# Performance work log

Measured on AMD Instinct MI355X. Metric: run time of the kernel, lower is better.

The kernel has to match this reference:

```python
import jax, jax.numpy as jnp
import numpy as np

N_E = 100000       # entities
N_R = 1000         # relations
N_CLASSES = 20000  # class_index.max() + 1
E = 1000000        # edges (triples)
E_HIDDEN = 256
C_HIDDEN = 128
R_HIDDEN = 128
NEG_SLOPE = 0.01   # F.leaky_relu default


def leaky_relu(x):
    return jnp.where(x >= 0, x, NEG_SLOPE * x)


def segment_softmax(x, idx, num_segments):
    # torch_geometric-style scatter softmax over segments given by idx
    m = jax.ops.segment_max(x, idx, num_segments=num_segments)
    ex = jnp.exp(x - m[idx])
    s = jax.ops.segment_sum(ex, idx, num_segments=num_segments)
    return ex / (s[idx] + 1e-16)


def setup_inputs() -> dict:
    key = jax.random.key(0)
    ks = jax.random.split(key, 20)
    inv_c = 1.0 / np.sqrt(C_HIDDEN)
    inv_r = 1.0 / np.sqrt(R_HIDDEN)
    inv_e = 1.0 / np.sqrt(E_HIDDEN)
    inp = {
        "x_e": jax.random.normal(ks[0], (N_E, E_HIDDEN), jnp.float32),
        "edge_index": jax.random.randint(ks[1], (2, E), 0, N_E),
        "rel": jax.random.randint(ks[2], (E,), 0, N_R),
        "triple_num": jax.random.randint(ks[3], (E,), 0, N_E),
        "r_emb": jax.random.normal(ks[4], (N_R, R_HIDDEN), jnp.float32),
        "class_index": jax.random.randint(ks[5], (E,), 0, N_CLASSES),
        "head_class": jax.random.randint(ks[6], (N_CLASSES,), 0, N_E),
        # attention projection vectors (Linear(c_hidden,1,bias=False) weights)
        "a_h1": jax.random.normal(ks[7], (C_HIDDEN,), jnp.float32) * inv_c,
        "a_h2": jax.random.normal(ks[8], (C_HIDDEN,), jnp.float32) * inv_c,
        "a_h3": jax.random.normal(ks[9], (C_HIDDEN,), jnp.float32) * inv_c,
        "a_h4": jax.random.normal(ks[10], (C_HIDDEN,), jnp.float32) * inv_c,
        "a_t1": jax.random.normal(ks[11], (C_HIDDEN,), jnp.float32) * inv_c,
        "a_t2": jax.random.normal(ks[12], (C_HIDDEN,), jnp.float32) * inv_c,
        "a_t3": jax.random.normal(ks[13], (C_HIDDEN,), jnp.float32) * inv_c,
        "a_r1": jax.random.normal(ks[14], (R_HIDDEN,), jnp.float32) * inv_r,
        "a_r2": jax.random.normal(ks[15], (R_HIDDEN,), jnp.float32) * inv_r,
        "a_c": jax.random.normal(ks[16], (C_HIDDEN,), jnp.float32) * inv_c,
        # entity->class-space projections [e_hidden, c_hidden]
        "w_h": jax.random.normal(ks[17], (E_HIDDEN, C_HIDDEN), jnp.float32) * inv_e,
        "w_t": jax.random.normal(ks[18], (E_HIDDEN, C_HIDDEN), jnp.float32) * inv_e,
        # highway gate Linear(c_hidden, c_hidden)
        "hw_w": jax.random.normal(ks[19], (C_HIDDEN, C_HIDDEN), jnp.float32) * inv_c,
        "hw_b": jnp.zeros((C_HIDDEN,), jnp.float32),
    }
    return inp


def reference(x_e, edge_index, rel, triple_num, r_emb, class_index, head_class,
              a_h1, a_h2, a_h3, a_h4, a_t1, a_t2, a_t3, a_r1, a_r2, a_c,
              w_h, w_t, hw_w, hw_b):
    h_idx = edge_index[0]
    t_idx = edge_index[1]

    x_r_h = jax.nn.relu(x_e @ w_h)   # [N_e, C]
    x_r_t = jax.nn.relu(x_e @ w_t)   # [N_e, C]

    # --- level 1: edge attention over triple_num segments ---
    e1 = ((x_r_h @ a_h1)[h_idx] + (x_r_t @ a_t1)[t_idx]) / 2 + (r_emb @ a_r1)[rel]
    alpha = segment_softmax(leaky_relu(e1), triple_num, N_E)       # [E]

    x_t = x_r_t[t_idx] * alpha[:, None]                            # [E, C]
    norm = jnp.linalg.norm(x_t, axis=1, keepdims=True)
    x_t = x_t / jnp.maximum(norm, 1e-12)                           # F.normalize p=2

    # --- level 2: relation/class attention over class_index segments ---
    e_t = x_t @ a_t2                                               # [E]
    e_h = (x_r_h @ a_h2)[h_idx]
    e_r = (r_emb @ a_r2)[rel]
    e_r = (e_r + ((x_r_h @ a_h3)[h_idx] + (x_t @ a_t3)) / 2) / 2
    beta = segment_softmax(leaky_relu(e_t + e_r + e_h), class_index, N_CLASSES)

    # spmm: A[class_index[i], t_idx[i]] = beta[i];  x_class = A @ x_t
    x_class = jax.ops.segment_sum(beta[:, None] * x_t[t_idx],
                                  class_index, num_segments=N_CLASSES)  # [N_CLASSES, C]

    # --- level 3: class->head-entity attention over head_class segments ---
    e_c = (x_class @ a_c) + (x_r_h @ a_h4)[head_class]             # [N_CLASSES]
    gama = segment_softmax(leaky_relu(e_c), head_class, N_E)
    x_e_h = jax.ops.segment_sum(gama[:, None] * x_class,
                                head_class, num_segments=N_E)      # [N_e, C]

    # highway combine
    gate = jax.nn.sigmoid(x_r_h @ hw_w + hw_b)
    return gate * x_e_h + (1.0 - gate) * x_r_h
```

## Files before the change

kernel.cpp:

```cpp
#include <hip/hip_runtime.h>
#include <hip/hip_bf16.h>

#define LRELU(x) ((x) >= 0.f ? (x) : 0.01f * (x))

typedef __attribute__((ext_vector_type(8))) short short8v;
typedef __attribute__((ext_vector_type(4))) float f32x4;

__device__ inline unsigned fenc(float x) {
    unsigned u = __float_as_uint(x);
    return (u & 0x80000000u) ? ~u : (u | 0x80000000u);
}
__device__ inline float fdec(unsigned e) {
    return __uint_as_float((e & 0x80000000u) ? (e ^ 0x80000000u) : ~e);
}

__device__ inline float wred(float v) {
#pragma unroll
    for (int o = 32; o > 0; o >>= 1) v += __shfl_xor(v, o, 64);
    return v;
}
__device__ inline float wredmax(float v) {
#pragma unroll
    for (int o = 32; o > 0; o >>= 1) v = fmaxf(v, __shfl_xor(v, o, 64));
    return v;
}

__device__ inline unsigned short f2bu(float x) {
    __hip_bfloat16 b = __float2bfloat16(x);
    return *reinterpret_cast<unsigned short*>(&b);
}
__device__ inline float bu2f(unsigned short u) {
    return __uint_as_float((unsigned)u << 16);
}

__device__ inline f32x4 mfma16(short8v a, short8v b, f32x4 c) {
    return __builtin_amdgcn_mfma_f32_16x16x32_bf16(a, b, c, 0, 0, 0);
}

__device__ inline void gload16(const void* g, void* l) {
    __builtin_amdgcn_global_load_lds(
        (const __attribute__((address_space(1))) void*)g,
        (__attribute__((address_space(3))) void*)l, 16, 0, 0);
}

__global__ __launch_bounds__(256) void k_prelude(
    const float* __restrict__ wh, const float* __restrict__ wt,
    const float* __restrict__ hww, unsigned short* __restrict__ wtb_hi,
    unsigned short* __restrict__ hwt_hi,
    const float* __restrict__ remb, const float* __restrict__ ar2,
    float* __restrict__ er2, int NR,
    const int* __restrict__ cidx, int* __restrict__ cnt, int E,
    int nbConv, int nbRel) {
    int bx = blockIdx.x, tid = threadIdx.x;
    if (bx < nbConv) {
        int id = bx * 256 + tid;
        if (id < 256 * 256) {
            int n = id >> 8, k = id & 255;
            float v = (n < 128) ? wh[(size_t)k * 128 + n]
                                : wt[(size_t)k * 128 + (n - 128)];
            wtb_hi[(size_t)n * 256 + k] = f2bu(v);
        } else {
            int id2 = id - 256 * 256;
            if (id2 < 128 * 128) {
                int n = id2 >> 7, k = id2 & 127;
                hwt_hi[(size_t)n * 128 + k] = f2bu(hww[(size_t)k * 128 + n]);
            }
        }
    } else if (bx < nbConv + nbRel) {
        int lane = tid & 63;
        int r = (bx - nbConv) * 4 + (tid >> 6);
        if (r >= NR) return;
        float v0 = remb[(size_t)r * 128 + lane];
        float v1 = remb[(size_t)r * 128 + 64 + lane];
        float p2 = wred(v0 * ar2[lane] + v1 * ar2[64 + lane]);
        if (lane == 0) er2[r] = p2;
    } else {
        int i = (bx - nbConv - nbRel) * 256 + tid;
        if (i >= E) return;
        atomicAdd(&cnt[cidx[i]], 1);
    }
}

__global__ __launch_bounds__(512) void k_mm_proj(
    const float* __restrict__ Af32, const unsigned short* __restrict__ Bh,
    unsigned short* __restrict__ oh0, unsigned short* __restrict__ oh1, int M,
    const float* __restrict__ ah2, const float* __restrict__ ah3,
    const float* __restrict__ ah4, const float* __restrict__ at2,
    const float* __restrict__ at3,
    float* __restrict__ hb, float* __restrict__ eh4o,
    float2* __restrict__ pta, const int* __restrict__ tidxg) {
    constexpr int KD = 256;
    constexpr int NSTEP = KD / 32;
    __shared__ float As_f[2][128 * 32];
    __shared__ unsigned short Bs_h[2][256 * 32];

    int row0 = blockIdx.x * 128;
    if (row0 + 128 > M) row0 = M - 128;
    int tid = threadIdx.x, w = tid >> 6, l = tid & 63;
    int rg = w & 3, ch = w >> 2;
    int lr = l & 15, hi4 = l >> 4;
    int srow = l >> 2, sslot = l & 3;
    int arow = l >> 3, afi = l & 7;

    f32x4 acc[2][8];
#pragma unroll
    for (int i = 0; i < 2; i++)
#pragma unroll
        for (int j = 0; j < 8; j++) acc[i][j] = (f32x4){0.f, 0.f, 0.f, 0.f};

    auto stage = [&](int s, int b) {
        int k0 = s * 32;
#pragma unroll
        for (int i = 0; i < 4; i++) {
            int u = w * 4 + i;
            if (u < 16) {
                int row = u * 8 + arow;
                int sf = ((afi ^ arow) << 2);
                gload16(Af32 + (size_t)(row0 + row) * KD + k0 + sf,
                        (char*)&As_f[b][0] + u * 1024);
            } else {
                int ub = u - 16;
                int n = ub * 16 + srow;
                int klog = (sslot ^ ((n >> 1) & 3)) * 8;
                gload16(Bh + (size_t)n * KD + k0 + klog,
                        (char*)&Bs_h[b][0] + ub * 1024);
            }
        }
    };

    stage(0, 0);
    __syncthreads();
    for (int s = 0; s < NSTEP; s++) {
        int b = s & 1;
        if (s + 1 < NSTEP) stage(s + 1, b ^ 1);

        short8v am_h[2];
#pragma unroll
        for (int mr = 0; mr < 2; mr++) {
            int r = rg * 32 + mr * 16 + lr;
            int s0 = ((2 * hi4 + 0) ^ (r & 7)) * 4;
            int s1 = ((2 * hi4 + 1) ^ (r & 7)) * 4;
            float4 f0 = *(const float4*)&As_f[b][r * 32 + s0];
            float4 f1 = *(const float4*)&As_f[b][r * 32 + s1];
            short8v v;
            v[0] = (short)f2bu(f0.x); v[1] = (short)f2bu(f0.y);
            v[2] = (short)f2bu(f0.z); v[3] = (short)f2bu(f0.w);
            v[4] = (short)f2bu(f1.x); v[5] = (short)f2bu(f1.y);
            v[6] = (short)f2bu(f1.z); v[7] = (short)f2bu(f1.w);
            am_h[mr] = v;
        }
#pragma unroll
        for (int ncc = 0; ncc < 8; ncc += 4) {
            short8v bn_h[4];
#pragma unroll
            for (int j = 0; j < 4; j++) {
                int n = ch * 128 + (ncc + j) * 16 + lr;
                int ko = (hi4 ^ ((n >> 1) & 3)) * 8;
                bn_h[j] = *(const short8v*)&Bs_h[b][n * 32 + ko];
            }
#pragma unroll
            for (int mr = 0; mr < 2; mr++)
#pragma unroll
                for (int j = 0; j < 4; j++)
                    acc[mr][ncc + j] = mfma16(am_h[mr], bn_h[j], acc[mr][ncc + j]);
        }
        __syncthreads();
    }

    unsigned short* OH = ch ? oh1 : oh0;
    const float* v1 = ch ? at2 : ah2;
    const float* v2 = ch ? at3 : ah3;
#pragma unroll
    for (int mr = 0; mr < 2; mr++)
#pragma unroll
        for (int rr = 0; rr < 4; rr++) {
            int row = row0 + rg * 32 + mr * 16 + hi4 * 4 + rr;
            float d0 = 0.f, d1 = 0.f, d2 = 0.f;
#pragma unroll
            for (int nc = 0; nc < 8; nc++) {
                float v = fmaxf(acc[mr][nc][rr], 0.f);
                int col = nc * 16 + lr;
                d0 = fmaf(v, v1[col], d0);
                d1 = fmaf(v, v2[col], d1);
                d2 = ch ? fmaf(v, v, d2) : fmaf(v, ah4[col], d2);
            }
#pragma unroll
            for (int o = 1; o <= 8; o <<= 1) {
                d0 += __shfl_xor(d0, o, 64);
                d1 += __shfl_xor(d1, o, 64);
                d2 += __shfl_xor(d2, o, 64);
            }
            float inv = 1.f;
            if (ch) inv = 1.f / fmaxf(sqrtf(d2), 1e-12f);
#pragma unroll
            for (int nc = 0; nc < 8; nc++) {
                float v = fmaxf(acc[mr][nc][rr], 0.f);
                OH[(size_t)row * 128 + nc * 16 + lr] = f2bu(ch ? v * inv : v);
            }
            if (lr == 0) {
                if (ch == 0) {
                    hb[row] = d0 + 0.25f * d1;
                    eh4o[row] = d2;
                } else {
                    float tav = (d0 + 0.25f * d1) * inv;
                    pta[row] = make_float2(tav, __int_as_float(tidxg[row]));
                }
            }
        }
}

__global__ __launch_bounds__(512) void k_mm_hw(
    const unsigned short* __restrict__ Ah, const unsigned short* __restrict__ Bh,
    float* __restrict__ o0, const float* __restrict__ bias,
    const float* __restrict__ xeh, const unsigned* __restrict__ m3f, int M) {
    constexpr int KD = 128;
    constexpr int NSTEP = KD / 32;
    __shared__ unsigned short As_h[2][256 * 32];
    __shared__ unsigned short Bs_h[2][128 * 32];

    int row0 = blockIdx.x * 256;
    if (row0 + 256 > M) row0 = M - 256;
    int tid = threadIdx.x, w = tid >> 6, l = tid & 63;
    int lr = l & 15, hi4 = l >> 4;
    int srow = l >> 2, sslot = l & 3;

    f32x4 acc[2][8];
#pragma unroll
    for (int i = 0; i < 2; i++)
#pragma unroll
        for (int j = 0; j < 8; j++) acc[i][j] = (f32x4){0.f, 0.f, 0.f, 0.f};

    auto stage = [&](int s, int b) {
        int k0 = s * 32;
#pragma unroll
        for (int i = 0; i < 3; i++) {
            int u = w * 3 + i;
            if (u < 16) {
                int row = u * 16 + srow;
                int klog = (sslot ^ ((row >> 1) & 3)) * 8;
                gload16(Ah + (size_t)(row0 + row) * KD + k0 + klog,
                        (char*)&As_h[b][0] + u * 1024);
            } else {
                int ub = u - 16;
                int row = ub * 16 + srow;
                int klog = (sslot ^ ((row >> 1) & 3)) * 8;
                gload16(Bh + (size_t)row * KD + k0 + klog,
                        (char*)&Bs_h[b][0] + ub * 1024);
            }
        }
    };

    stage(0, 0);
    __syncthreads();
    for (int s = 0; s < NSTEP; s++) {
        int b = s & 1;
        if (s + 1 < NSTEP) stage(s + 1, b ^ 1);
        short8v am_h[2];
#pragma unroll
        for (int mr = 0; mr < 2; mr++) {
            int r = w * 32 + mr * 16 + lr;
            int ko = (hi4 ^ ((r >> 1) & 3)) * 8;
            am_h[mr] = *(const short8v*)&As_h[b][r * 32 + ko];
        }
#pragma unroll
        for (int ncc = 0; ncc < 8; ncc += 4) {
            short8v bn_h[4];
#pragma unroll
            for (int j = 0; j < 4; j++) {
                int n = (ncc + j) * 16 + lr;
                int ko = (hi4 ^ ((n >> 1) & 3)) * 8;
                bn_h[j] = *(const short8v*)&Bs_h[b][n * 32 + ko];
            }
#pragma unroll
            for (int mr = 0; mr < 2; mr++)
#pragma unroll
                for (int j = 0; j < 4; j++)
                    acc[mr][ncc + j] = mfma16(am_h[mr], bn_h[j], acc[mr][ncc + j]);
        }
        __syncthreads();
    }

#pragma unroll
    for (int mr = 0; mr < 2; mr++)
#pragma unroll
        for (int rr = 0; rr < 4; rr++) {
            int row = row0 + w * 32 + mr * 16 + hi4 * 4 + rr;
            bool touched = (m3f[row] != 0u);
#pragma unroll
            for (int nc = 0; nc < 8; nc++) {
                int col = nc * 16 + lr;
                float a = acc[mr][nc][rr] + bias[col];
                float g = 1.f / (1.f + expf(-a));
                size_t o = (size_t)row * 128 + col;
                float af = bu2f(Ah[o]);
                float xv = 0.f;
                if (touched) xv = xeh[o];
                o0[o] = g * xv + (1.f - g) * af;
            }
        }
}

__global__ __launch_bounds__(1024) void k_scan(const int* __restrict__ cnt,
                                               int* __restrict__ off,
                                               int* __restrict__ cur, int NC) {
    __shared__ int wt[16];
    __shared__ int sbase;
    int tid = threadIdx.x, w = tid >> 6, lane = tid & 63;
    if (tid == 0) sbase = 0;
    __syncthreads();
    for (int c0 = 0; c0 < NC; c0 += 1024) {
        int c = c0 + tid;
        int v = (c < NC) ? cnt[c] : 0;
        int x = v;
#pragma unroll
        for (int o = 1; o < 64; o <<= 1) {
            int t = __shfl_up(x, o, 64);
            if (lane >= o) x += t;
        }
        if (lane == 63) wt[w] = x;
        __syncthreads();
        int pre = 0, tot = 0;
#pragma unroll
        for (int i = 0; i < 16; i++) {
            int t = wt[i];
            tot += t;
            if (i < w) pre += t;
        }
        int excl = sbase + pre + x - v;
        if (c < NC) { off[c] = excl; cur[c] = excl; }
        __syncthreads();
        if (tid == 0) sbase += tot;
        __syncthreads();
    }
}

__global__ __launch_bounds__(256) void k_edgescatter(
    const int* __restrict__ cidx, int* __restrict__ cur,
    const int* __restrict__ hidx, const int* __restrict__ tidx,
    const int* __restrict__ rel, const float2* __restrict__ pta,
    const float* __restrict__ hb, const float* __restrict__ er2,
    float2* __restrict__ e2gs, int E) {
    int i = blockIdx.x * 256 + threadIdx.x;
    if (i >= E) return;
    int pos = atomicAdd(&cur[cidx[i]], 1);
    float2 p = pta[tidx[i]];
    float z2 = p.x + hb[hidx[i]] + 0.5f * er2[rel[i]];
    e2gs[pos] = make_float2(LRELU(z2), p.y);
}

__global__ __launch_bounds__(256) void k_spmm2(
    const int* __restrict__ off, const int* __restrict__ cnt,
    const float2* __restrict__ e2gs, const unsigned* __restrict__ xrtn_b,
    float* __restrict__ xclass, const float* __restrict__ ac,
    const float* __restrict__ eh4, const int* __restrict__ hclass,
    float* __restrict__ zc, unsigned* __restrict__ m3, int NC) {
    int lane = threadIdx.x & 63;
    int c = blockIdx.x * 4 + (threadIdx.x >> 6);
    if (c >= NC) return;
    int n = cnt[c];
    float a0 = 0.f, a1 = 0.f;
    if (n > 0) {
        int base = off[c];
        float m = -3.4e38f, s = 0.f;
        for (int j = lane; j < n; j += 64) {
            float z = e2gs[base + j].x;
            if (z > m) { s = s * __expf(m - z) + 1.f; m = z; }
            else s += __expf(z - m);
        }
        float M = wredmax(m);
        s = wred(s * __expf(m - M));
        float inv = 1.f / (s + 1e-16f);
        for (int j0 = 0; j0 < n; j0 += 64) {
            int lim = n - j0;
            if (lim > 64) lim = 64;
            float wv = 0.f;
            int g = 0;
            if (lane < lim) {
                float2 pg = e2gs[base + j0 + lane];
                wv = __expf(pg.x - M) * inv;
                g = __float_as_int(pg.y);
            }
            int jj = 0;
            for (; jj + 8 <= lim; jj += 8) {
                float w0 = __shfl(wv, jj + 0), w1 = __shfl(wv, jj + 1);
                float w2 = __shfl(wv, jj + 2), w3 = __shfl(wv, jj + 3);
                float w4 = __shfl(wv, jj + 4), w5 = __shfl(wv, jj + 5);
                float w6 = __shfl(wv, jj + 6), w7 = __shfl(wv, jj + 7);
                unsigned u0 = xrtn_b[(size_t)__shfl(g, jj + 0) * 64 + lane];
                unsigned u1 = xrtn_b[(size_t)__shfl(g, jj + 1) * 64 + lane];
                unsigned u2 = xrtn_b[(size_t)__shfl(g, jj + 2) * 64 + lane];
                unsigned u3 = xrtn_b[(size_t)__shfl(g, jj + 3) * 64 + lane];
                unsigned u4 = xrtn_b[(size_t)__shfl(g, jj + 4) * 64 + lane];
                unsigned u5 = xrtn_b[(size_t)__shfl(g, jj + 5) * 64 + lane];
                unsigned u6 = xrtn_b[(size_t)__shfl(g, jj + 6) * 64 + lane];
                unsigned u7 = xrtn_b[(size_t)__shfl(g, jj + 7) * 64 + lane];
                a0 = fmaf(w0, bu2f((unsigned short)(u0 & 0xffff)), a0);
                a1 = fmaf(w0, bu2f((unsigned short)(u0 >> 16)), a1);
                a0 = fmaf(w1, bu2f((unsigned short)(u1 & 0xffff)), a0);
                a1 = fmaf(w1, bu2f((unsigned short)(u1 >> 16)), a1);
                a0 = fmaf(w2, bu2f((unsigned short)(u2 & 0xffff)), a0);
                a1 = fmaf(w2, bu2f((unsigned short)(u2 >> 16)), a1);
                a0 = fmaf(w3, bu2f((unsigned short)(u3 & 0xffff)), a0);
                a1 = fmaf(w3, bu2f((unsigned short)(u3 >> 16)), a1);
                a0 = fmaf(w4, bu2f((unsigned short)(u4 & 0xffff)), a0);
                a1 = fmaf(w4, bu2f((unsigned short)(u4 >> 16)), a1);
                a0 = fmaf(w5, bu2f((unsigned short)(u5 & 0xffff)), a0);
                a1 = fmaf(w5, bu2f((unsigned short)(u5 >> 16)), a1);
                a0 = fmaf(w6, bu2f((unsigned short)(u6 & 0xffff)), a0);
                a1 = fmaf(w6, bu2f((unsigned short)(u6 >> 16)), a1);
                a0 = fmaf(w7, bu2f((unsigned short)(u7 & 0xffff)), a0);
                a1 = fmaf(w7, bu2f((unsigned short)(u7 >> 16)), a1);
            }
            for (; jj < lim; jj++) {
                float wj = __shfl(wv, jj);
                unsigned u = xrtn_b[(size_t)__shfl(g, jj) * 64 + lane];
                a0 = fmaf(wj, bu2f((unsigned short)(u & 0xffff)), a0);
                a1 = fmaf(wj, bu2f((unsigned short)(u >> 16)), a1);
            }
        }
    }
    *(float2*)&xclass[(size_t)c * 128 + 2 * lane] = make_float2(a0, a1);
    float p = wred(a0 * ac[2 * lane] + a1 * ac[2 * lane + 1]);
    if (lane == 0) {
        int hc = hclass[c];
        float z = LRELU(p + eh4[hc]);
        zc[c] = z;
        atomicMax(&m3[hc], fenc(z));
    }
}

__global__ __launch_bounds__(256) void k_class2(
    const int* __restrict__ hclass, float* __restrict__ zc,
    const unsigned* __restrict__ m3, float* __restrict__ s3,
    float* __restrict__ xeh, int NC) {
    int lane = threadIdx.x & 63;
    int c = blockIdx.x * 4 + (threadIdx.x >> 6);
    if (c >= NC) return;
    int hc = hclass[c];
    *(float2*)&xeh[(size_t)hc * 128 + 2 * lane] = make_float2(0.f, 0.f);
    if (lane == 0) {
        float ex = expf(zc[c] - fdec(m3[hc]));
        zc[c] = ex;
        atomicAdd(&s3[hc], ex);
    }
}

__global__ __launch_bounds__(256) void k_class3(
    const int* __restrict__ hclass, const float* __restrict__ zc,
    const float* __restrict__ s3, const float* __restrict__ xclass,
    float* __restrict__ xeh, int NC) {
    int lane = threadIdx.x & 63;
    int c = blockIdx.x * 4 + (threadIdx.x >> 6);
    if (c >= NC) return;
    int hc = hclass[c];
    float gama = zc[c] / (s3[hc] + 1e-16f);
    float v0 = xclass[(size_t)c * 128 + lane], v1 = xclass[(size_t)c * 128 + 64 + lane];
    atomicAdd(&xeh[(size_t)hc * 128 + lane], gama * v0);
    atomicAdd(&xeh[(size_t)hc * 128 + 64 + lane], gama * v1);
}

extern "C" void kernel_launch(void* const* d_in, const int* in_sizes, int n_in,
                              void* d_out, int out_size, void* d_ws, size_t ws_size,
                              hipStream_t stream) {
    (void)n_in; (void)out_size; (void)ws_size;
    const float* xe   = (const float*)d_in[0];
    const int*   eidx = (const int*)d_in[1];
    const int*   rel  = (const int*)d_in[2];
    const float* remb = (const float*)d_in[4];
    const int*   cidx = (const int*)d_in[5];
    const int*   hcls = (const int*)d_in[6];
    const float* ah2  = (const float*)d_in[8];
    const float* ah3  = (const float*)d_in[9];
    const float* ah4  = (const float*)d_in[10];
    const float* at2  = (const float*)d_in[12];
    const float* at3  = (const float*)d_in[13];
    const float* ar2  = (const float*)d_in[15];
    const float* ac   = (const float*)d_in[16];
    const float* wh   = (const float*)d_in[17];
    const float* wt   = (const float*)d_in[18];
    const float* hww  = (const float*)d_in[19];
    const float* hwb  = (const float*)d_in[20];
    float* out = (float*)d_out;

    const int NE = in_sizes[0] / 256;
    const int E  = in_sizes[2];
    const int NR = in_sizes[4] / 128;
    const int NC = in_sizes[6];
    const int* hidx = eidx;
    const int* tidx = eidx + E;

    char* base = (char*)d_ws;
    size_t off0 = 0;
    auto alloc = [&](size_t bytes) -> char* {
        char* r = base + off0;
        off0 = (off0 + bytes + 255) & ~(size_t)255;
        return r;
    };
    float* hb   = (float*)alloc((size_t)NE * 4);
    float* eh4b = (float*)alloc((size_t)NE * 4);
    float2* pta = (float2*)alloc((size_t)NE * 8);
    float* er2b = (float*)alloc((size_t)NR * 4);
    float2* e2gs = (float2*)alloc((size_t)E * 8);
    float* zc   = (float*)alloc((size_t)NC * 4);
    unsigned short* wtb_hi = (unsigned short*)alloc((size_t)256 * 256 * 2);
    unsigned short* hwt_hi = (unsigned short*)alloc((size_t)128 * 128 * 2);
    unsigned short* xrh_hi = (unsigned short*)alloc((size_t)NE * 128 * 2);
    unsigned short* xrtn   = (unsigned short*)alloc((size_t)NE * 128 * 2);
    int* offb = (int*)alloc((size_t)NC * 4);
    int* curb = (int*)alloc((size_t)NC * 4);
    float* xclass = (float*)alloc((size_t)NC * 128 * 4);
    float* xeh    = (float*)alloc((size_t)NE * 128 * 4);
    size_t zoff = off0;
    unsigned* m3 = (unsigned*)alloc((size_t)NE * 4);
    float* s3    = (float*)alloc((size_t)NE * 4);
    int* cntb    = (int*)alloc((size_t)NC * 4);
    size_t zbytes = off0 - zoff;

    hipMemsetAsync(base + zoff, 0, zbytes, stream);

    int nbConv = (256 * 256 + 128 * 128 + 255) / 256;
    int nbRel  = (NR + 3) / 4;
    int nbHist = (E + 255) / 256;
    k_prelude<<<nbConv + nbRel + nbHist, 256, 0, stream>>>(
        wh, wt, hww, wtb_hi, hwt_hi, remb, ar2, er2b, NR, cidx, cntb, E,
        nbConv, nbRel);

    k_mm_proj<<<(NE + 127) / 128, 512, 0, stream>>>(
        xe, wtb_hi, xrh_hi, xrtn, NE,
        ah2, ah3, ah4, at2, at3, hb, eh4b, pta, tidx);

    k_scan<<<1, 1024, 0, stream>>>(cntb, offb, curb, NC);

    k_edgescatter<<<(E + 255) / 256, 256, 0, stream>>>(
        cidx, curb, hidx, tidx, rel, pta, hb, er2b, e2gs, E);

    k_spmm2<<<(NC + 3) / 4, 256, 0, stream>>>(offb, cntb, e2gs,
                                              (const unsigned*)xrtn, xclass,
                                              ac, eh4b, hcls, zc, m3, NC);
    k_class2<<<(NC + 3) / 4, 256, 0, stream>>>(hcls, zc, m3, s3, xeh, NC);
    k_class3<<<(NC + 3) / 4, 256, 0, stream>>>(hcls, zc, s3, xclass, xeh, NC);

    k_mm_hw<<<(NE + 255) / 256, 512, 0, stream>>>(
        xrh_hi, hwt_hi, out, hwb, xeh, m3, NE);
}
```

Before: 260.6 us.

## Convert A tile to bf16 once via registers; unroll class gather by 16

```diff
diff --git a/kernel.cpp b/kernel.cpp
--- a/kernel.cpp
+++ b/kernel.cpp
@@ -91,7 +91,7 @@
     float2* __restrict__ pta, const int* __restrict__ tidxg) {
     constexpr int KD = 256;
     constexpr int NSTEP = KD / 32;
-    __shared__ float As_f[2][128 * 32];
+    __shared__ unsigned short As_h[2][128 * 32];
     __shared__ unsigned short Bs_h[2][256 * 32];
 
     int row0 = blockIdx.x * 128;
@@ -100,7 +100,9 @@
     int rg = w & 3, ch = w >> 2;
     int lr = l & 15, hi4 = l >> 4;
     int srow = l >> 2, sslot = l & 3;
-    int arow = l >> 3, afi = l & 7;
+    int arow = tid >> 2, asg = tid & 3;
+    int asgl = asg ^ ((arow >> 1) & 3);
+    float4 rA0, rA1;
 
     f32x4 acc[2][8];
 #pragma unroll
@@ -108,46 +110,48 @@
 #pragma unroll
         for (int j = 0; j < 8; j++) acc[i][j] = (f32x4){0.f, 0.f, 0.f, 0.f};
 
-    auto stage = [&](int s, int b) {
+    auto loadA = [&](int s) {
+        const float* p = Af32 + (size_t)(row0 + arow) * KD + s * 32 + asgl * 8;
+        rA0 = *(const float4*)p;
+        rA1 = *(const float4*)(p + 4);
+    };
+    auto writeA = [&](int b) {
+        short8v v;
+        v[0] = (short)f2bu(rA0.x); v[1] = (short)f2bu(rA0.y);
+        v[2] = (short)f2bu(rA0.z); v[3] = (short)f2bu(rA0.w);
+        v[4] = (short)f2bu(rA1.x); v[5] = (short)f2bu(rA1.y);
+        v[6] = (short)f2bu(rA1.z); v[7] = (short)f2bu(rA1.w);
+        *(short8v*)&As_h[b][arow * 32 + asg * 8] = v;
+    };
+    auto stageB = [&](int s, int b) {
         int k0 = s * 32;
 #pragma unroll
-        for (int i = 0; i < 4; i++) {
-            int u = w * 4 + i;
-            if (u < 16) {
-                int row = u * 8 + arow;
-                int sf = ((afi ^ arow) << 2);
-                gload16(Af32 + (size_t)(row0 + row) * KD + k0 + sf,
-                        (char*)&As_f[b][0] + u * 1024);
-            } else {
-                int ub = u - 16;
-                int n = ub * 16 + srow;
-                int klog = (sslot ^ ((n >> 1) & 3)) * 8;
-                gload16(Bh + (size_t)n * KD + k0 + klog,
-                        (char*)&Bs_h[b][0] + ub * 1024);
-            }
+        for (int i = 0; i < 2; i++) {
+            int ub = w * 2 + i;
+            int n = ub * 16 + srow;
+            int klog = (sslot ^ ((n >> 1) & 3)) * 8;
+            gload16(Bh + (size_t)n * KD + k0 + klog,
+                    (char*)&Bs_h[b][0] + ub * 1024);
         }
     };
 
-    stage(0, 0);
+    loadA(0);
+    stageB(0, 0);
+    writeA(0);
     __syncthreads();
     for (int s = 0; s < NSTEP; s++) {
         int b = s & 1;
-        if (s + 1 < NSTEP) stage(s + 1, b ^ 1);
+        if (s + 1 < NSTEP) {
+            loadA(s + 1);
+            stageB(s + 1, b ^ 1);
+        }
 
         short8v am_h[2];
 #pragma unroll
         for (int mr = 0; mr < 2; mr++) {
             int r = rg * 32 + mr * 16 + lr;
-            int s0 = ((2 * hi4 + 0) ^ (r & 7)) * 4;
-            int s1 = ((2 * hi4 + 1) ^ (r & 7)) * 4;
-            float4 f0 = *(const float4*)&As_f[b][r * 32 + s0];
-            float4 f1 = *(const float4*)&As_f[b][r * 32 + s1];
-            short8v v;
-            v[0] = (short)f2bu(f0.x); v[1] = (short)f2bu(f0.y);
-            v[2] = (short)f2bu(f0.z); v[3] = (short)f2bu(f0.w);
-            v[4] = (short)f2bu(f1.x); v[5] = (short)f2bu(f1.y);
-            v[6] = (short)f2bu(f1.z); v[7] = (short)f2bu(f1.w);
-            am_h[mr] = v;
+            int ko = (hi4 ^ ((r >> 1) & 3)) * 8;
+            am_h[mr] = *(const short8v*)&As_h[b][r * 32 + ko];
         }
 #pragma unroll
         for (int ncc = 0; ncc < 8; ncc += 4) {
@@ -164,6 +168,7 @@
                 for (int j = 0; j < 4; j++)
                     acc[mr][ncc + j] = mfma16(am_h[mr], bn_h[j], acc[mr][ncc + j]);
         }
+        if (s + 1 < NSTEP) writeA(b ^ 1);
         __syncthreads();
     }
 
@@ -381,35 +386,41 @@
                 g = __float_as_int(pg.y);
             }
             int jj = 0;
+            for (; jj + 16 <= lim; jj += 16) {
+                float w16[16];
+                int g16[16];
+#pragma unroll
+                for (int q = 0; q < 16; q++) {
+                    w16[q] = __shfl(wv, jj + q);
+                    g16[q] = __shfl(g, jj + q);
+                }
+                unsigned u16[16];
+#pragma unroll
+                for (int q = 0; q < 16; q++)
+                    u16[q] = xrtn_b[(size_t)g16[q] * 64 + lane];
+#pragma unroll
+                for (int q = 0; q < 16; q++) {
+                    a0 = fmaf(w16[q], bu2f((unsigned short)(u16[q] & 0xffff)), a0);
+                    a1 = fmaf(w16[q], bu2f((unsigned short)(u16[q] >> 16)), a1);
+                }
+            }
             for (; jj + 8 <= lim; jj += 8) {
-                float w0 = __shfl(wv, jj + 0), w1 = __shfl(wv, jj + 1);
-                float w2 = __shfl(wv, jj + 2), w3 = __shfl(wv, jj + 3);
-                float w4 = __shfl(wv, jj + 4), w5 = __shfl(wv, jj + 5);
-                float w6 = __shfl(wv, jj + 6), w7 = __shfl(wv, jj + 7);
-                unsigned u0 = xrtn_b[(size_t)__shfl(g, jj + 0) * 64 + lane];
-                unsigned u1 = xrtn_b[(size_t)__shfl(g, jj + 1) * 64 + lane];
-                unsigned u2 = xrtn_b[(size_t)__shfl(g, jj + 2) * 64 + lane];
-                unsigned u3 = xrtn_b[(size_t)__shfl(g, jj + 3) * 64 + lane];
-                unsigned u4 = xrtn_b[(size_t)__shfl(g, jj + 4) * 64 + lane];
-                unsigned u5 = xrtn_b[(size_t)__shfl(g, jj + 5) * 64 + lane];
-                unsigned u6 = xrtn_b[(size_t)__shfl(g, jj + 6) * 64 + lane];
-                unsigned u7 = xrtn_b[(size_t)__shfl(g, jj + 7) * 64 + lane];
-                a0 = fmaf(w0, bu2f((unsigned short)(u0 & 0xffff)), a0);
-                a1 = fmaf(w0, bu2f((unsigned short)(u0 >> 16)), a1);
-                a0 = fmaf(w1, bu2f((unsigned short)(u1 & 0xffff)), a0);
-                a1 = fmaf(w1, bu2f((unsigned short)(u1 >> 16)), a1);
-                a0 = fmaf(w2, bu2f((unsigned short)(u2 & 0xffff)), a0);
-                a1 = fmaf(w2, bu2f((unsigned short)(u2 >> 16)), a1);
-                a0 = fmaf(w3, bu2f((unsigned short)(u3 & 0xffff)), a0);
-                a1 = fmaf(w3, bu2f((unsigned short)(u3 >> 16)), a1);
-                a0 = fmaf(w4, bu2f((unsigned short)(u4 & 0xffff)), a0);
-                a1 = fmaf(w4, bu2f((unsigned short)(u4 >> 16)), a1);
-                a0 = fmaf(w5, bu2f((unsigned short)(u5 & 0xffff)), a0);
-                a1 = fmaf(w5, bu2f((unsigned short)(u5 >> 16)), a1);
-                a0 = fmaf(w6, bu2f((unsigned short)(u6 & 0xffff)), a0);
-                a1 = fmaf(w6, bu2f((unsigned short)(u6 >> 16)), a1);
-                a0 = fmaf(w7, bu2f((unsigned short)(u7 & 0xffff)), a0);
-                a1 = fmaf(w7, bu2f((unsigned short)(u7 >> 16)), a1);
+                float w8[8];
+                int g8[8];
+#pragma unroll
+                for (int q = 0; q < 8; q++) {
+                    w8[q] = __shfl(wv, jj + q);
+                    g8[q] = __shfl(g, jj + q);
+                }
+                unsigned u8[8];
+#pragma unroll
+                for (int q = 0; q < 8; q++)
+                    u8[q] = xrtn_b[(size_t)g8[q] * 64 + lane];
+#pragma unroll
+                for (int q = 0; q < 8; q++) {
+                    a0 = fmaf(w8[q], bu2f((unsigned short)(u8[q] & 0xffff)), a0);
+                    a1 = fmaf(w8[q], bu2f((unsigned short)(u8[q] >> 16)), a1);
+                }
             }
             for (; jj < lim; jj++) {
                 float wj = __shfl(wv, jj);
```

New measurement: 264.9 us. Within noise of the previous version (+1.6%).
